# Optimization experiments

Hardware: AMD Instinct MI355X
Metric: run time of the kernel (lower is better)

## Reference

```python
import jax, jax.numpy as jnp
import numpy as np

B, S, HID = 2, 2048, 1024
H, KVH, HD = 16, 8, 64
KEEP, RATIO = 1024, 0.7
SCALE = HD ** -0.5
NEG = -1e9  # additive causal mask value (finite to avoid -inf + finfo.min overflow)


def setup_inputs() -> dict:
    key = jax.random.key(0)
    ks = jax.random.split(key, 8)
    hidden_states = jax.random.normal(ks[0], (B, S, HID), jnp.float32)
    # standard RoPE tables, shape [B, S, HD]
    inv_freq = 1.0 / (10000.0 ** (np.arange(0, HD, 2, dtype=np.float32) / HD))
    freqs = np.outer(np.arange(S, dtype=np.float32), inv_freq)      # [S, HD/2]
    emb = np.concatenate([freqs, freqs], axis=-1)                    # [S, HD]
    cos = jnp.broadcast_to(jnp.asarray(np.cos(emb))[None], (B, S, HD)).astype(jnp.float32)
    sin = jnp.broadcast_to(jnp.asarray(np.sin(emb))[None], (B, S, HD)).astype(jnp.float32)
    # additive causal attention mask [B, 1, S, S]
    causal = np.where(np.tril(np.ones((S, S), dtype=bool)), 0.0, NEG).astype(np.float32)
    attention_mask = jnp.broadcast_to(jnp.asarray(causal)[None, None], (B, 1, S, S))
    w = 0.02
    Wq = jax.random.normal(ks[1], (H * HD, HID), jnp.float32) * w
    Wk = jax.random.normal(ks[2], (KVH * HD, HID), jnp.float32) * w
    Wv = jax.random.normal(ks[3], (KVH * HD, HID), jnp.float32) * w
    A = jax.random.normal(ks[4], (H,), jnp.float32) * 0.1
    Wdt = jax.random.normal(ks[5], (H, KVH * HD), jnp.float32) * w
    Wo = jax.random.normal(ks[6], (HID, H * HD), jnp.float32) * w
    return {"hidden_states": hidden_states, "cos": cos, "sin": sin,
            "attention_mask": attention_mask, "Wq": Wq, "Wk": Wk, "Wv": Wv,
            "A": A, "Wdt": Wdt, "Wo": Wo}


def _rotate_half(x):
    return jnp.concatenate([-x[..., HD // 2:], x[..., :HD // 2]], axis=-1)


def reference(hidden_states, cos, sin, attention_mask, Wq, Wk, Wv, A, Wdt, Wo):
    # projections -> [B, heads, S, HD]
    q = (hidden_states @ Wq.T).reshape(B, S, H, HD).transpose(0, 2, 1, 3)
    k = (hidden_states @ Wk.T).reshape(B, S, KVH, HD).transpose(0, 2, 1, 3)
    v = (hidden_states @ Wv.T).reshape(B, S, KVH, HD).transpose(0, 2, 1, 3)
    # RoPE (cos/sin broadcast over heads)
    c, s = cos[:, None], sin[:, None]
    q = q * c + _rotate_half(q) * s
    k = k * c + _rotate_half(k) * s
    # dynamic mask from values: dt_proj(softplus) -> exp(A * ...)
    dt = v.transpose(0, 2, 1, 3).reshape(B, S, KVH * HD) @ Wdt.T            # [B, S, H]
    dyn = jnp.exp(A * jax.nn.softplus(dt)).transpose(0, 2, 1)               # [B, H, S]
    m = dyn[:, :, None, :]                                                  # [B, H, 1, S]
    # top-k style thresholding: mask everything below the kth smallest value
    kth = int((S - KEEP) * RATIO)                                           # = 716 here
    rate = jnp.sort(m, axis=-1)[..., kth - 1:kth]                           # kthvalue, keepdim
    min_val = jnp.finfo(hidden_states.dtype).min
    m = jnp.where(m < rate, min_val, m)
    m = m + attention_mask                                                  # [B, H, S, S]
    # GQA: repeat kv heads
    g = H // KVH
    kf = jnp.repeat(k, g, axis=1)
    vf = jnp.repeat(v, g, axis=1)
    scores = jnp.einsum('bhqd,bhkd->bhqk', q, kf) * SCALE + m
    attn = jax.nn.softmax(scores, axis=-1)
    out = jnp.einsum('bhqk,bhkd->bhqd', attn, vf)
    out = out.transpose(0, 2, 1, 3).reshape(B, S, H * HD)
    return out @ Wo.T
```

## Files before the change

kernel.cpp:

```cpp
#include <hip/hip_runtime.h>
#include <hip/hip_bf16.h>


typedef __attribute__((ext_vector_type(8))) short bf16x8;
typedef __attribute__((ext_vector_type(4))) float f32x4;

#define FMIN (-3.4028234663852886e38f)
#define M_FIX 24.0f

__device__ __forceinline__ short bf16s(float x) {
  __hip_bfloat16 h = __float2bfloat16(x);
  return __builtin_bit_cast(short, h);
}
__device__ __forceinline__ float bf16f(short s) {
  return __bfloat162float(__builtin_bit_cast(__hip_bfloat16, s));
}

__device__ __forceinline__ void gload_lds16(const void* g, void* l) {
  __builtin_amdgcn_global_load_lds(
      (__attribute__((address_space(1))) void*)(void*)(g),
      (__attribute__((address_space(3))) void*)(l), 16, 0, 0);
}

__global__ void cvt_all(const float* __restrict__ hsrc, const float* __restrict__ wq,
                        const float* __restrict__ wk, const float* __restrict__ wv,
                        const float* __restrict__ wo, __hip_bfloat16* __restrict__ hb,
                        __hip_bfloat16* __restrict__ wqkv, __hip_bfloat16* __restrict__ wob) {
  int i = blockIdx.x * 256 + threadIdx.x;
  const float4* src;
  ushort4* dst;
  int off;
  if (i < 1048576) { src = (const float4*)hsrc; dst = (ushort4*)hb; off = i; }
  else if (i < 1310720) { src = (const float4*)wq; dst = (ushort4*)wqkv; off = i - 1048576; }
  else if (i < 1441792) { src = (const float4*)wk; dst = (ushort4*)wqkv + 262144; off = i - 1310720; }
  else if (i < 1572864) { src = (const float4*)wv; dst = (ushort4*)wqkv + 393216; off = i - 1441792; }
  else { src = (const float4*)wo; dst = (ushort4*)wob; off = i - 1572864; }
  float4 v = src[off];
  ushort4 o;
  o.x = (unsigned short)bf16s(v.x);
  o.y = (unsigned short)bf16s(v.y);
  o.z = (unsigned short)bf16s(v.z);
  o.w = (unsigned short)bf16s(v.w);
  dst[off] = o;
}

__global__ void wcomb_kernel(const float* __restrict__ Wdt, const float* __restrict__ Wv,
                             float* __restrict__ Wcomb) {
  int t = blockIdx.x * 256 + threadIdx.x;
  int h = t >> 10, c = t & 1023;
  float acc = 0.f;
#pragma unroll 4
  for (int d4 = 0; d4 < 512; d4 += 4) {
    float4 wd = *reinterpret_cast<const float4*>(Wdt + h * 512 + d4);
    acc = fmaf(wd.x, Wv[(size_t)(d4 + 0) * 1024 + c], acc);
    acc = fmaf(wd.y, Wv[(size_t)(d4 + 1) * 1024 + c], acc);
    acc = fmaf(wd.z, Wv[(size_t)(d4 + 2) * 1024 + c], acc);
    acc = fmaf(wd.w, Wv[(size_t)(d4 + 3) * 1024 + c], acc);
  }
  Wcomb[t] = acc;
}

__global__ void dyn_kernel(const float* __restrict__ hidden, const float* __restrict__ Wcomb,
                           const float* __restrict__ A, float* __restrict__ dyn) {
  int t = blockIdx.x * 256 + threadIdx.x;
  int bs = t >> 4, h = t & 15;
  const float4* hv = reinterpret_cast<const float4*>(hidden + (size_t)bs * 1024);
  const float4* wv = reinterpret_cast<const float4*>(Wcomb + (size_t)h * 1024);
  float acc = 0.f;
#pragma unroll 8
  for (int c = 0; c < 256; ++c) {
    float4 a = hv[c], b = wv[c];
    acc += a.x * b.x + a.y * b.y + a.z * b.z + a.w * b.w;
  }
  float sp = fmaxf(acc, 0.f) + log1pf(expf(-fabsf(acc)));
  float dv = expf(A[h] * sp);
  int b = bs >> 11, s = bs & 2047;
  dyn[(((size_t)(b * 16 + h)) << 11) + s] = dv;
}

__global__ void rate_kernel(const float* __restrict__ dyn, float* __restrict__ rate) {
  __shared__ unsigned int hist[256];
  __shared__ unsigned int scan[256];
  __shared__ unsigned int sh_prefix, sh_rank;
  const int bh = blockIdx.x, t = threadIdx.x;
  const unsigned int* src = (const unsigned int*)(dyn + ((size_t)bh << 11));
  if (t == 0) { sh_prefix = 0u; sh_rank = 716u; }
  __syncthreads();
  for (int pass = 0; pass < 4; ++pass) {
    const int shift = 24 - 8 * pass;
    hist[t] = 0u;
    __syncthreads();
    const unsigned int pfx = sh_prefix;
    const unsigned int mask = (pass == 0) ? 0u : (0xFFFFFFFFu << (shift + 8));
    const unsigned int rank = sh_rank;
    for (int i = t; i < 2048; i += 256) {
      unsigned int u = src[i];
      if ((u & mask) == pfx) atomicAdd(&hist[(u >> shift) & 255], 1u);
    }
    __syncthreads();
    unsigned int v = hist[t];
    scan[t] = v;
    __syncthreads();
    for (int o = 1; o < 256; o <<= 1) {
      unsigned int add = (t >= o) ? scan[t - o] : 0u;
      __syncthreads();
      scan[t] += add;
      __syncthreads();
    }
    unsigned int cum = scan[t];
    unsigned int prev = (t > 0) ? scan[t - 1] : 0u;
    if (prev < rank && rank <= cum) {
      sh_prefix = pfx | ((unsigned int)t << shift);
      sh_rank = rank - prev;
    }
    __syncthreads();
  }
  if (t == 0) rate[bh] = __uint_as_float(sh_prefix);
}

template <int MODE>
__global__ __launch_bounds__(256) void gemm_bt(
    const __hip_bfloat16* __restrict__ A, const __hip_bfloat16* __restrict__ Bm,
    float* __restrict__ Cout,
    __hip_bfloat16* __restrict__ Qb, __hip_bfloat16* __restrict__ Kb,
    __hip_bfloat16* __restrict__ Vt,
    const float* __restrict__ cosp, const float* __restrict__ sinp,
    int M, int N, int K) {
  __shared__ __hip_bfloat16 Al[128 * 32];
  __shared__ __hip_bfloat16 Bl[128 * 32];
  const int nb = N >> 7;
  const int bm = blockIdx.x / nb, bn = blockIdx.x % nb;
  const int m0 = bm << 7, n0 = bn << 7;
  const int tid = threadIdx.x, lane = tid & 63, w = tid >> 6;
  const int wr = w >> 1, wc = w & 1;
  const int lg = lane >> 4, li = lane & 15;
  f32x4 acc[4][4] = {};
  for (int k0 = 0; k0 < K; k0 += 32) {
    __syncthreads();
#pragma unroll
    for (int i = 0; i < 2; ++i) {
      int ci = i * 256 + w * 64 + lane;
      int row = ci >> 2, c8 = (ci & 3) << 3;
      gload_lds16(A + (size_t)(m0 + row) * K + k0 + c8, Al + (size_t)(i * 256 + w * 64) * 8);
      gload_lds16(Bm + (size_t)(n0 + row) * K + k0 + c8, Bl + (size_t)(i * 256 + w * 64) * 8);
    }
    __syncthreads();
    bf16x8 af[4], bfr[4];
#pragma unroll
    for (int f = 0; f < 4; ++f) {
      af[f] = *reinterpret_cast<const bf16x8*>(Al + (wr * 64 + f * 16 + li) * 32 + lg * 8);
      bfr[f] = *reinterpret_cast<const bf16x8*>(Bl + (wc * 64 + f * 16 + li) * 32 + lg * 8);
    }
#pragma unroll
    for (int fm = 0; fm < 4; ++fm)
#pragma unroll
      for (int fn = 0; fn < 4; ++fn)
        acc[fm][fn] = __builtin_amdgcn_mfma_f32_16x16x32_bf16(af[fm], bfr[fn], acc[fm][fn], 0, 0, 0);
  }
  if constexpr (MODE == 1) {
#pragma unroll
    for (int fm = 0; fm < 4; ++fm)
#pragma unroll
      for (int fn = 0; fn < 4; ++fn) {
        int col = n0 + wc * 64 + fn * 16 + li;
#pragma unroll
        for (int j = 0; j < 4; ++j) {
          int row = m0 + wr * 64 + fm * 16 + lg * 4 + j;
          Cout[(size_t)row * N + col] = acc[fm][fn][j];
        }
      }
  } else {
    const int n0w = n0 + wc * 64;
#pragma unroll
    for (int fm = 0; fm < 4; ++fm)
#pragma unroll
      for (int j = 0; j < 4; ++j) {
        int r = m0 + wr * 64 + fm * 16 + lg * 4 + j;
        int b = r >> 11, s = r & 2047;
        if (n0w < 1536) {
#pragma unroll
          for (int fn = 0; fn < 4; ++fn) {
            int d = fn * 16 + li;
            float cv = cosp[(size_t)r * 64 + d];
            float sv = sinp[(size_t)r * 64 + d];
            float x = acc[fm][fn][j];
            float rot = (fn < 2) ? -acc[fm][fn + 2][j] : acc[fm][fn - 2][j];
            __hip_bfloat16 hv = __float2bfloat16(x * cv + rot * sv);
            if (n0w < 1024) {
              int h = n0w >> 6;
              Qb[(((size_t)(b * 16 + h) << 11) + s) * 64 + d] = hv;
            } else {
              int kvh = (n0w - 1024) >> 6;
              Kb[(((size_t)(b * 8 + kvh) << 11) + s) * 64 + d] = hv;
            }
          }
        } else {
          int kvh = (n0w - 1536) >> 6;
#pragma unroll
          for (int fn = 0; fn < 4; ++fn) {
            int d = fn * 16 + li;
            Vt[((size_t)(b * 8 + kvh) * 64 + d) * 2048 + s] = __float2bfloat16(acc[fm][fn][j]);
          }
        }
      }
  }
}

__global__ __launch_bounds__(256, 2) void attn_kernel(
    const __hip_bfloat16* __restrict__ Qb, const __hip_bfloat16* __restrict__ Kb,
    const __hip_bfloat16* __restrict__ Vt, const float* __restrict__ dyn,
    const float* __restrict__ rate, __hip_bfloat16* __restrict__ AO) {
  __shared__ __hip_bfloat16 Klds[2][4096];
  __shared__ __hip_bfloat16 Vlds[2][4096];
  __shared__ short Pl[4][1024];
  const int orig = blockIdx.x;
  const int bid = ((orig & 7) << 6) + (orig >> 3);
  const int pr = bid & 15, h = (bid >> 4) & 15, b = bid >> 8;
  const int qtA = pr, qtB = 31 - pr;
  const int kvh = h >> 1;
  const int tid = threadIdx.x, lane = tid & 63, w = tid >> 6;
  const int lg = lane >> 4, li = lane & 15;
  const int q0A = qtA * 64 + w * 16, q0B = qtB * 64 + w * 16;
  const __hip_bfloat16* Qp = Qb + ((size_t)(b * 16 + h) << 11) * 64;
  const __hip_bfloat16* Kp = Kb + ((size_t)(b * 8 + kvh) << 11) * 64;
  const __hip_bfloat16* Vp = Vt + ((size_t)(b * 8 + kvh) << 17);
  const float* dynp = dyn + ((size_t)(b * 16 + h) << 11);
  const float rt = rate[b * 16 + h];
  bf16x8 qaA0 = *reinterpret_cast<const bf16x8*>(Qp + (size_t)(q0A + li) * 64 + lg * 8);
  bf16x8 qaA1 = *reinterpret_cast<const bf16x8*>(Qp + (size_t)(q0A + li) * 64 + 32 + lg * 8);
  bf16x8 qaB0 = *reinterpret_cast<const bf16x8*>(Qp + (size_t)(q0B + li) * 64 + lg * 8);
  bf16x8 qaB1 = *reinterpret_cast<const bf16x8*>(Qp + (size_t)(q0B + li) * 64 + 32 + lg * 8);
  f32x4 oaA[4] = {}, oaB[4] = {};
  float lpA[4] = {0.f, 0.f, 0.f, 0.f}, lpB[4] = {0.f, 0.f, 0.f, 0.f};
  int qrA[4], qrB[4];
#pragma unroll
  for (int j = 0; j < 4; ++j) { qrA[j] = q0A + lg * 4 + j; qrB[j] = q0B + lg * 4 + j; }
  short* pl = &Pl[w][0];
  const int kc_end = qtB + 1;

  const int srow = (tid >> 3), sseg = tid & 7;
  const int ssw = (sseg ^ (srow & 7)) * 8;

  auto stage = [&](int buf, int kc) {
    const size_t k0 = (size_t)kc * 64;
#pragma unroll
    for (int it = 0; it < 2; ++it) {
      int row = it * 32 + srow;
      gload_lds16(Kp + (k0 + row) * 64 + ssw, &Klds[buf][(it * 256 + w * 64) * 8]);
      gload_lds16(Vp + (size_t)row * 2048 + k0 + ssw, &Vlds[buf][(it * 256 + w * 64) * 8]);
    }
  };

  auto computeTile = [&](const bf16x8& qf0, const bf16x8& qf1, f32x4 (&oa)[4],
                         float (&lp)[4], const int (&qr)[4],
                         const bf16x8 (&kb)[4][2], const bf16x8 (&vb)[2][4],
                         const float (&dv)[4], int k0) {
    f32x4 sf[4];
#pragma unroll
    for (int cf = 0; cf < 4; ++cf) {
      f32x4 z = {};
      z = __builtin_amdgcn_mfma_f32_16x16x32_bf16(qf0, kb[cf][0], z, 0, 0, 0);
      z = __builtin_amdgcn_mfma_f32_16x16x32_bf16(qf1, kb[cf][1], z, 0, 0, 0);
      sf[cf] = z;
    }
#pragma unroll
    for (int cf = 0; cf < 4; ++cf) {
      int kk = k0 + cf * 16 + li;
      float mv = (dv[cf] < rt) ? FMIN : dv[cf];
#pragma unroll
      for (int j = 0; j < 4; ++j) {
        float sc = sf[cf][j] * 0.125f + mv;
        sc = (kk > qr[j]) ? sc - 1e9f : sc;
        float p = __expf(sc - M_FIX);
        lp[j] += p;
        int r = lg * 4 + j;
        int e = (r << 6) + cf * 16 + li;
        e ^= (r & 7) << 3;
        pl[e] = bf16s(p);
      }
    }
#pragma unroll
    for (int m2 = 0; m2 < 2; ++m2) {
      int e = (li << 6) + m2 * 32 + lg * 8;
      e ^= (li & 7) << 3;
      bf16x8 pa = *reinterpret_cast<const bf16x8*>(pl + e);
#pragma unroll
      for (int df = 0; df < 4; ++df)
        oa[df] = __builtin_amdgcn_mfma_f32_16x16x32_bf16(pa, vb[m2][df], oa[df], 0, 0, 0);
    }
  };

  int buf = 0;
  stage(0, 0);
  __syncthreads();
  for (int kc = 0; kc < kc_end; ++kc) {
    if (kc + 1 < kc_end) stage(buf ^ 1, kc + 1);
    const int k0 = kc * 64;
    float dv[4];
#pragma unroll
    for (int cf = 0; cf < 4; ++cf) dv[cf] = dynp[k0 + cf * 16 + li];
    const int rsw = li & 7;
    bf16x8 kb[4][2];
#pragma unroll
    for (int cf = 0; cf < 4; ++cf)
#pragma unroll
      for (int half = 0; half < 2; ++half)
        kb[cf][half] = *reinterpret_cast<const bf16x8*>(
            &Klds[buf][(cf * 16 + li) * 64 + ((half * 4 + lg) ^ rsw) * 8]);
    bf16x8 vb[2][4];
#pragma unroll
    for (int m2 = 0; m2 < 2; ++m2)
#pragma unroll
      for (int df = 0; df < 4; ++df)
        vb[m2][df] = *reinterpret_cast<const bf16x8*>(
            &Vlds[buf][(df * 16 + li) * 64 + ((m2 * 4 + lg) ^ rsw) * 8]);
    computeTile(qaB0, qaB1, oaB, lpB, qrB, kb, vb, dv, k0);
    if (kc <= qtA) computeTile(qaA0, qaA1, oaA, lpA, qrA, kb, vb, dv, k0);
    __syncthreads();
    buf ^= 1;
  }

#pragma unroll
  for (int off = 1; off < 16; off <<= 1)
#pragma unroll
    for (int j = 0; j < 4; ++j) {
      lpA[j] += __shfl_xor(lpA[j], off);
      lpB[j] += __shfl_xor(lpB[j], off);
    }

#pragma unroll
  for (int df = 0; df < 4; ++df)
#pragma unroll
    for (int j = 0; j < 4; ++j) {
      int d = df * 16 + li;
      float lA = lpA[j], lB = lpB[j];
      float oA = (lA > 0.f) ? oaA[df][j] / lA : 0.f;
      float oB = (lB > 0.f) ? oaB[df][j] / lB : 0.f;
      int qA = q0A + lg * 4 + j, qB = q0B + lg * 4 + j;
      AO[((size_t)((b << 11) + qA)) * 1024 + (h << 6) + d] = __float2bfloat16(oA);
      AO[((size_t)((b << 11) + qB)) * 1024 + (h << 6) + d] = __float2bfloat16(oB);
    }
}

__global__ __launch_bounds__(1024) void fixup_kernel(const __hip_bfloat16* __restrict__ Vt,
                                                     const float* __restrict__ dyn,
                                                     const float* __restrict__ rate,
                                                     __hip_bfloat16* __restrict__ AO) {
  __shared__ float maskAll[2048];
  __shared__ float partial[16][64];
  __shared__ float cnt_slice[16];
  __shared__ float totd[64];
  __shared__ float pre[64][64];
  __shared__ float cntp[64];
  __shared__ float CntSh;
  const int bh = blockIdx.x;
  const int b = bh >> 4, h = bh & 15, kvh = h >> 1;
  const float rt = rate[bh];
  const float* dynp = dyn + ((size_t)bh << 11);
  const __hip_bfloat16* Vp = Vt + ((size_t)(b * 8 + kvh) << 17);
  const int t = threadIdx.x;
  for (int i = t; i < 2048; i += 1024) maskAll[i] = (dynp[i] >= rt) ? 1.f : 0.f;
  __syncthreads();
  const int d = t & 63, ks = t >> 6;
  {
    const __hip_bfloat16* vrow = Vp + (size_t)d * 2048 + ks * 128;
    float sum = 0.f;
#pragma unroll 4
    for (int kk = 0; kk < 128; kk += 8) {
      bf16x8 v8 = *reinterpret_cast<const bf16x8*>(vrow + kk);
      const float* mp = &maskAll[ks * 128 + kk];
#pragma unroll
      for (int j = 0; j < 8; ++j) sum += mp[j] * bf16f(v8[j]);
    }
    partial[ks][d] = sum;
    if (d == 0) {
      float c = 0.f;
      for (int k = ks * 128; k < ks * 128 + 128; ++k) c += maskAll[k];
      cnt_slice[ks] = c;
    }
  }
  __syncthreads();
  if (t < 64) {
    float s2 = 0.f;
#pragma unroll
    for (int ksi = 0; ksi < 16; ++ksi) s2 += partial[ksi][t];
    totd[t] = s2;
  } else if (t == 64) {
    float c = 0.f;
#pragma unroll
    for (int i = 0; i < 16; ++i) c += cnt_slice[i];
    CntSh = c;
  } else if (t == 65) {
    float run = 0.f;
    for (int k = 0; k < 64; ++k) { run += maskAll[k]; cntp[k] = run; }
  } else if (t >= 128 && t < 192) {
    int dd = t - 128;
    const __hip_bfloat16* vr = Vp + (size_t)dd * 2048;
    float run = 0.f;
    for (int k = 0; k < 64; ++k) {
      run += maskAll[k] * __bfloat162float(vr[k]);
      pre[k][dd] = run;
    }
  }
  __syncthreads();
  const float Cnt = CntSh;
  for (int idx = t; idx < 4096; idx += 1024) {
    int q = idx >> 6, dd = idx & 63;
    if (cntp[q] == 0.f) {
      float val = (totd[dd] - pre[q][dd]) / (Cnt - cntp[q]);
      AO[((size_t)((b << 11) + q)) * 1024 + (h << 6) + dd] = __float2bfloat16(val);
    }
  }
}

extern "C" void kernel_launch(void* const* d_in, const int* in_sizes, int n_in,
                              void* d_out, int out_size, void* d_ws, size_t ws_size,
                              hipStream_t stream) {
  const float* hidden = (const float*)d_in[0];
  const float* cosp   = (const float*)d_in[1];
  const float* sinp   = (const float*)d_in[2];
  const float* Wq  = (const float*)d_in[4];
  const float* Wk  = (const float*)d_in[5];
  const float* Wv  = (const float*)d_in[6];
  const float* Av  = (const float*)d_in[7];
  const float* Wdt = (const float*)d_in[8];
  const float* Wo  = (const float*)d_in[9];
  float* out = (float*)d_out;

  char* ws = (char*)d_ws;
  size_t off = 0;
  auto alloc = [&](size_t bytes) {
    char* p = ws + off;
    off += (bytes + 255) & ~(size_t)255;
    return (void*)p;
  };
  __hip_bfloat16* hb   = (__hip_bfloat16*)alloc(4096ULL * 1024 * 2);
  __hip_bfloat16* wqkv = (__hip_bfloat16*)alloc(2048ULL * 1024 * 2);
  __hip_bfloat16* wob  = (__hip_bfloat16*)alloc(1024ULL * 1024 * 2);
  __hip_bfloat16* Qb   = (__hip_bfloat16*)alloc(2ULL * 16 * 2048 * 64 * 2);
  __hip_bfloat16* Kb   = (__hip_bfloat16*)alloc(2ULL * 8 * 2048 * 64 * 2);
  __hip_bfloat16* Vt   = (__hip_bfloat16*)alloc(2ULL * 8 * 2048 * 64 * 2);
  float* wcomb = (float*)alloc(16ULL * 1024 * 4);
  float* dynb  = (float*)alloc(2ULL * 16 * 2048 * 4);
  float* rateb = (float*)alloc(256);
  __hip_bfloat16* ao = (__hip_bfloat16*)alloc(4096ULL * 1024 * 2);

  cvt_all<<<7168, 256, 0, stream>>>(hidden, Wq, Wk, Wv, Wo, hb, wqkv, wob);
  wcomb_kernel<<<64, 256, 0, stream>>>(Wdt, Wv, wcomb);
  gemm_bt<0><<<512, 256, 0, stream>>>(hb, wqkv, nullptr, Qb, Kb, Vt, cosp, sinp,
                                      4096, 2048, 1024);
  dyn_kernel<<<256, 256, 0, stream>>>(hidden, wcomb, Av, dynb);
  rate_kernel<<<32, 256, 0, stream>>>(dynb, rateb);
  attn_kernel<<<512, 256, 0, stream>>>(Qb, Kb, Vt, dynb, rateb, ao);
  fixup_kernel<<<32, 1024, 0, stream>>>(Vt, dynb, rateb, ao);
  gemm_bt<1><<<256, 256, 0, stream>>>(ao, wob, out, nullptr, nullptr, nullptr,
                                      nullptr, nullptr, 4096, 1024, 1024);
}
```

Before: 312.0 us.

## Fuse prep kernels, warp-scan rate histogram, swizzle GEMM grid, precompute mask in LDS

The bf16 conversion and Wcomb computation now run in a single launch, and the Wcomb dot product is split across four slices and reduced in shared memory. The rate kernel replaces its LDS Hillis-Steele scan with wavefront shuffle scans plus a small cross-wave add. The GEMM block index is remapped with an XCD-style swizzle, and the attention kernel precomputes the thresholded, offset dynamic mask into LDS once per block. The causal compare is applied only on diagonal tiles. These are several unrelated tweaks aimed at launch overhead, barriers and per-tile ALU work, at the cost of 8KB more LDS in the attention kernel, which may affect occupancy.

Result: faster. 298.1 us (-4.5%).

```diff
diff --git a/kernel.cpp b/kernel.cpp
--- a/kernel.cpp
+++ b/kernel.cpp
@@ -22,42 +22,47 @@
       (__attribute__((address_space(3))) void*)(l), 16, 0, 0);
 }
 
-__global__ void cvt_all(const float* __restrict__ hsrc, const float* __restrict__ wq,
-                        const float* __restrict__ wk, const float* __restrict__ wv,
-                        const float* __restrict__ wo, __hip_bfloat16* __restrict__ hb,
-                        __hip_bfloat16* __restrict__ wqkv, __hip_bfloat16* __restrict__ wob) {
-  int i = blockIdx.x * 256 + threadIdx.x;
-  const float4* src;
-  ushort4* dst;
-  int off;
-  if (i < 1048576) { src = (const float4*)hsrc; dst = (ushort4*)hb; off = i; }
-  else if (i < 1310720) { src = (const float4*)wq; dst = (ushort4*)wqkv; off = i - 1048576; }
-  else if (i < 1441792) { src = (const float4*)wk; dst = (ushort4*)wqkv + 262144; off = i - 1310720; }
-  else if (i < 1572864) { src = (const float4*)wv; dst = (ushort4*)wqkv + 393216; off = i - 1441792; }
-  else { src = (const float4*)wo; dst = (ushort4*)wob; off = i - 1572864; }
-  float4 v = src[off];
-  ushort4 o;
-  o.x = (unsigned short)bf16s(v.x);
-  o.y = (unsigned short)bf16s(v.y);
-  o.z = (unsigned short)bf16s(v.z);
-  o.w = (unsigned short)bf16s(v.w);
-  dst[off] = o;
-}
-
-__global__ void wcomb_kernel(const float* __restrict__ Wdt, const float* __restrict__ Wv,
-                             float* __restrict__ Wcomb) {
-  int t = blockIdx.x * 256 + threadIdx.x;
-  int h = t >> 10, c = t & 1023;
-  float acc = 0.f;
-#pragma unroll 4
-  for (int d4 = 0; d4 < 512; d4 += 4) {
-    float4 wd = *reinterpret_cast<const float4*>(Wdt + h * 512 + d4);
-    acc = fmaf(wd.x, Wv[(size_t)(d4 + 0) * 1024 + c], acc);
-    acc = fmaf(wd.y, Wv[(size_t)(d4 + 1) * 1024 + c], acc);
-    acc = fmaf(wd.z, Wv[(size_t)(d4 + 2) * 1024 + c], acc);
-    acc = fmaf(wd.w, Wv[(size_t)(d4 + 3) * 1024 + c], acc);
-  }
-  Wcomb[t] = acc;
+__global__ void prep_kernel(const float* __restrict__ hsrc, const float* __restrict__ wq,
+                            const float* __restrict__ wk, const float* __restrict__ wv,
+                            const float* __restrict__ wo, const float* __restrict__ Wdt,
+                            __hip_bfloat16* __restrict__ hb, __hip_bfloat16* __restrict__ wqkv,
+                            __hip_bfloat16* __restrict__ wob, float* __restrict__ Wcomb) {
+  __shared__ float part[4][64];
+  const int blk = blockIdx.x;
+  if (blk < 7168) {
+    int i = blk * 256 + threadIdx.x;
+    const float4* src;
+    ushort4* dst;
+    int off;
+    if (i < 1048576) { src = (const float4*)hsrc; dst = (ushort4*)hb; off = i; }
+    else if (i < 1310720) { src = (const float4*)wq; dst = (ushort4*)wqkv; off = i - 1048576; }
+    else if (i < 1441792) { src = (const float4*)wk; dst = (ushort4*)wqkv + 262144; off = i - 1310720; }
+    else if (i < 1572864) { src = (const float4*)wv; dst = (ushort4*)wqkv + 393216; off = i - 1441792; }
+    else { src = (const float4*)wo; dst = (ushort4*)wob; off = i - 1572864; }
+    float4 v = src[off];
+    ushort4 o;
+    o.x = (unsigned short)bf16s(v.x);
+    o.y = (unsigned short)bf16s(v.y);
+    o.z = (unsigned short)bf16s(v.z);
+    o.w = (unsigned short)bf16s(v.w);
+    dst[off] = o;
+  } else {
+    const int t = threadIdx.x;
+    const int out = (blk - 7168) * 64 + (t & 63);
+    const int slice = t >> 6;
+    const int h = out >> 10, c = out & 1023;
+    const float* wd = Wdt + h * 512 + slice * 128;
+    const float* wvp = wv + (size_t)(slice * 128) * 1024 + c;
+    float acc = 0.f;
+#pragma unroll 8
+    for (int i = 0; i < 128; ++i) acc = fmaf(wd[i], wvp[(size_t)i * 1024], acc);
+    part[slice][t & 63] = acc;
+    __syncthreads();
+    if (t < 64) {
+      float s = ((part[0][t] + part[1][t]) + part[2][t]) + part[3][t];
+      Wcomb[(blk - 7168) * 64 + t] = s;
+    }
+  }
 }
 
 __global__ void dyn_kernel(const float* __restrict__ hidden, const float* __restrict__ Wcomb,
@@ -80,9 +85,10 @@
 
 __global__ void rate_kernel(const float* __restrict__ dyn, float* __restrict__ rate) {
   __shared__ unsigned int hist[256];
-  __shared__ unsigned int scan[256];
+  __shared__ unsigned int wsum[4];
   __shared__ unsigned int sh_prefix, sh_rank;
   const int bh = blockIdx.x, t = threadIdx.x;
+  const int lane = t & 63, w = t >> 6;
   const unsigned int* src = (const unsigned int*)(dyn + ((size_t)bh << 11));
   if (t == 0) { sh_prefix = 0u; sh_rank = 716u; }
   __syncthreads();
@@ -91,24 +97,25 @@
     hist[t] = 0u;
     __syncthreads();
     const unsigned int pfx = sh_prefix;
+    const unsigned int rank = sh_rank;
     const unsigned int mask = (pass == 0) ? 0u : (0xFFFFFFFFu << (shift + 8));
-    const unsigned int rank = sh_rank;
     for (int i = t; i < 2048; i += 256) {
       unsigned int u = src[i];
       if ((u & mask) == pfx) atomicAdd(&hist[(u >> shift) & 255], 1u);
     }
     __syncthreads();
     unsigned int v = hist[t];
-    scan[t] = v;
-    __syncthreads();
-    for (int o = 1; o < 256; o <<= 1) {
-      unsigned int add = (t >= o) ? scan[t - o] : 0u;
-      __syncthreads();
-      scan[t] += add;
-      __syncthreads();
-    }
-    unsigned int cum = scan[t];
-    unsigned int prev = (t > 0) ? scan[t - 1] : 0u;
+    unsigned int s = v;
+#pragma unroll
+    for (int o = 1; o < 64; o <<= 1) {
+      unsigned int n = __shfl_up(s, o);
+      if (lane >= o) s += n;
+    }
+    if (lane == 63) wsum[w] = s;
+    __syncthreads();
+    unsigned int offs = 0;
+    for (int i2 = 0; i2 < w; ++i2) offs += wsum[i2];
+    unsigned int cum = s + offs, prev = cum - v;
     if (prev < rank && rank <= cum) {
       sh_prefix = pfx | ((unsigned int)t << shift);
       sh_rank = rank - prev;
@@ -129,7 +136,10 @@
   __shared__ __hip_bfloat16 Al[128 * 32];
   __shared__ __hip_bfloat16 Bl[128 * 32];
   const int nb = N >> 7;
-  const int bm = blockIdx.x / nb, bn = blockIdx.x % nb;
+  const int nbx = gridDim.x >> 3;
+  const int orig = blockIdx.x;
+  const int bidg = (orig & 7) * nbx + (orig >> 3);
+  const int bm = bidg / nb, bn = bidg % nb;
   const int m0 = bm << 7, n0 = bn << 7;
   const int tid = threadIdx.x, lane = tid & 63, w = tid >> 6;
   const int wr = w >> 1, wc = w & 1;
@@ -213,6 +223,7 @@
   __shared__ __hip_bfloat16 Klds[2][4096];
   __shared__ __hip_bfloat16 Vlds[2][4096];
   __shared__ short Pl[4][1024];
+  __shared__ float Dm[2048];
   const int orig = blockIdx.x;
   const int bid = ((orig & 7) << 6) + (orig >> 3);
   const int pr = bid & 15, h = (bid >> 4) & 15, b = bid >> 8;
@@ -254,7 +265,7 @@
   auto computeTile = [&](const bf16x8& qf0, const bf16x8& qf1, f32x4 (&oa)[4],
                          float (&lp)[4], const int (&qr)[4],
                          const bf16x8 (&kb)[4][2], const bf16x8 (&vb)[2][4],
-                         const float (&dv)[4], int k0) {
+                         const float (&dmv)[4], int k0, bool diag) {
     f32x4 sf[4];
 #pragma unroll
     for (int cf = 0; cf < 4; ++cf) {
@@ -266,12 +277,11 @@
 #pragma unroll
     for (int cf = 0; cf < 4; ++cf) {
       int kk = k0 + cf * 16 + li;
-      float mv = (dv[cf] < rt) ? FMIN : dv[cf];
 #pragma unroll
       for (int j = 0; j < 4; ++j) {
-        float sc = sf[cf][j] * 0.125f + mv;
-        sc = (kk > qr[j]) ? sc - 1e9f : sc;
-        float p = __expf(sc - M_FIX);
+        float sc = fmaf(sf[cf][j], 0.125f, dmv[cf]);
+        if (diag) sc = (kk > qr[j]) ? sc - 1e9f : sc;
+        float p = __expf(sc);
         lp[j] += p;
         int r = lg * 4 + j;
         int e = (r << 6) + cf * 16 + li;
@@ -290,15 +300,19 @@
     }
   };
 
+  for (int i = tid; i < 2048; i += 256) {
+    float dv = dynp[i];
+    Dm[i] = (dv < rt) ? FMIN : dv - M_FIX;
+  }
   int buf = 0;
   stage(0, 0);
   __syncthreads();
   for (int kc = 0; kc < kc_end; ++kc) {
     if (kc + 1 < kc_end) stage(buf ^ 1, kc + 1);
     const int k0 = kc * 64;
-    float dv[4];
-#pragma unroll
-    for (int cf = 0; cf < 4; ++cf) dv[cf] = dynp[k0 + cf * 16 + li];
+    float dmv[4];
+#pragma unroll
+    for (int cf = 0; cf < 4; ++cf) dmv[cf] = Dm[k0 + cf * 16 + li];
     const int rsw = li & 7;
     bf16x8 kb[4][2];
 #pragma unroll
@@ -314,8 +328,10 @@
       for (int df = 0; df < 4; ++df)
         vb[m2][df] = *reinterpret_cast<const bf16x8*>(
             &Vlds[buf][(df * 16 + li) * 64 + ((m2 * 4 + lg) ^ rsw) * 8]);
-    computeTile(qaB0, qaB1, oaB, lpB, qrB, kb, vb, dv, k0);
-    if (kc <= qtA) computeTile(qaA0, qaA1, oaA, lpA, qrA, kb, vb, dv, k0);
+    if (kc < qtB) computeTile(qaB0, qaB1, oaB, lpB, qrB, kb, vb, dmv, k0, false);
+    else          computeTile(qaB0, qaB1, oaB, lpB, qrB, kb, vb, dmv, k0, true);
+    if (kc < qtA)       computeTile(qaA0, qaA1, oaA, lpA, qrA, kb, vb, dmv, k0, false);
+    else if (kc == qtA) computeTile(qaA0, qaA1, oaA, lpA, qrA, kb, vb, dmv, k0, true);
     __syncthreads();
     buf ^= 1;
   }
@@ -445,8 +461,7 @@
   float* rateb = (float*)alloc(256);
   __hip_bfloat16* ao = (__hip_bfloat16*)alloc(4096ULL * 1024 * 2);
 
-  cvt_all<<<7168, 256, 0, stream>>>(hidden, Wq, Wk, Wv, Wo, hb, wqkv, wob);
-  wcomb_kernel<<<64, 256, 0, stream>>>(Wdt, Wv, wcomb);
+  prep_kernel<<<7424, 256, 0, stream>>>(hidden, Wq, Wk, Wv, Wo, Wdt, hb, wqkv, wob, wcomb);
   gemm_bt<0><<<512, 256, 0, stream>>>(hb, wqkv, nullptr, Qb, Kb, Vt, cosp, sinp,
                                       4096, 2048, 1024);
   dyn_kernel<<<256, 256, 0, stream>>>(hidden, wcomb, Av, dynb);
```
